# Kernel optimization log

Hardware: AMD Instinct MI355X
Metric: run time of the kernel (lower is better)

The kernel has to match this reference:

```python
import jax, jax.numpy as jnp
import numpy as np

OUT_CHANNELS = 16
IN_CHANNELS = 16
EPS = 1e-8
NEG_SLOPE = 0.1


def setup_inputs() -> dict:
    key = jax.random.key(0)
    k1, _ = jax.random.split(key)
    x = jax.random.normal(k1, (16, IN_CHANNELS, 512, 512), dtype=jnp.float32)
    # default weight from the torch module: pattern - 0.01, flattened to [16]
    pattern = jnp.array([0, 1, 0, 0, 1, 0, 0, 1, 0, 0, 1, 0, 0, 1, 0, 0], dtype=jnp.float32)
    w = pattern - 0.01
    b = jnp.zeros((1,), dtype=jnp.float32)
    return {"x": x, "w": w, "b": b}


def reference(x, w, b):
    # Rolled 1x1 conv: out[:, o] = sum_c w[(c - o) % Cin] * x[:, c] + b
    # (since _roll_tensor(x, o)[c] = x[(c + o) % Cin])
    W2 = jnp.stack([jnp.roll(w, o) for o in range(OUT_CHANNELS)])  # [O, C] circulant
    y = jnp.einsum('bchw,oc->bohw', x, W2) + b[0]
    # leaky_relu(0.1)
    y = jnp.where(y >= 0, y, NEG_SLOPE * y)
    # per (batch, channel) min-max normalize over spatial dims
    mn = jnp.min(y, axis=(2, 3), keepdims=True)
    mx = jnp.max(y, axis=(2, 3), keepdims=True)
    return (y - mn) / (mx - mn + EPS)
```

## Files before the change

kernel.cpp:

```cpp
#include <hip/hip_runtime.h>
#include <math.h>

static constexpr int NB = 16;
static constexpr int NC = 16;
static constexpr int HW = 512 * 512;
static constexpr int V4 = HW / 4;
static constexpr int THREADS = 256;
static constexpr int BLK_PER_B = 128;
static constexpr int ITERS = V4 / (BLK_PER_B * THREADS);
static constexpr int GRID = NB * BLK_PER_B;
static constexpr float NEG_SLOPE = 0.1f;
static constexpr float EPS = 1e-8f;

__device__ __forceinline__ unsigned int fenc(float f) {
    unsigned int u = __float_as_uint(f);
    return (u & 0x80000000u) ? ~u : (u | 0x80000000u);
}
__device__ __forceinline__ float fdec(unsigned int u) {
    u = (u & 0x80000000u) ? (u ^ 0x80000000u) : ~u;
    return __uint_as_float(u);
}

__device__ __forceinline__ float leaky(float v) {
    return v >= 0.0f ? v : NEG_SLOPE * v;
}

template<int PASS>
__global__ __launch_bounds__(THREADS)
void cc_kernel(const float* __restrict__ x, const float* __restrict__ w,
               const float* __restrict__ bptr, unsigned int* __restrict__ mnmx,
               float* __restrict__ out)
{
    const int blk = (PASS == 0) ? blockIdx.x : (GRID - 1 - (int)blockIdx.x);
    const int batch = blk >> 7;
    const int chunk = blk & (BLK_PER_B - 1);
    const float* xb = x + (size_t)batch * NC * HW;

    float wr[16];
    #pragma unroll
    for (int i = 0; i < 16; ++i) wr[i] = w[i];
    const float bias = bptr[0];

    __shared__ float smn[16];
    __shared__ float sscale[16];
    float mn[16], mx[16];

    if (PASS == 0) {
        #pragma unroll
        for (int o = 0; o < 16; ++o) { mn[o] = INFINITY; mx[o] = -INFINITY; }
    } else {
        if (threadIdx.x < 16) {
            const float mnv = fdec(mnmx[batch * 16 + threadIdx.x]);
            const float mxv = fdec(mnmx[256 + batch * 16 + threadIdx.x]);
            smn[threadIdx.x] = mnv;
            sscale[threadIdx.x] = 1.0f / (mxv - mnv + EPS);
        }
        __syncthreads();
    }

    #pragma unroll
    for (int it = 0; it < ITERS; ++it) {
        const int p4 = chunk * (THREADS * ITERS) + it * THREADS + (int)threadIdx.x;
        float4 acc[16];
        #pragma unroll
        for (int o = 0; o < 16; ++o) acc[o] = make_float4(bias, bias, bias, bias);
        #pragma unroll
        for (int c = 0; c < 16; ++c) {
            const float4 xv = reinterpret_cast<const float4*>(xb + (size_t)c * HW)[p4];
            #pragma unroll
            for (int o = 0; o < 16; ++o) {
                const float wc = wr[(c - o) & 15];
                acc[o].x = fmaf(wc, xv.x, acc[o].x);
                acc[o].y = fmaf(wc, xv.y, acc[o].y);
                acc[o].z = fmaf(wc, xv.z, acc[o].z);
                acc[o].w = fmaf(wc, xv.w, acc[o].w);
            }
        }
        #pragma unroll
        for (int o = 0; o < 16; ++o) {
            float4 v = acc[o];
            v.x = leaky(v.x); v.y = leaky(v.y); v.z = leaky(v.z); v.w = leaky(v.w);
            if (PASS == 0) {
                mn[o] = fminf(mn[o], fminf(fminf(v.x, v.y), fminf(v.z, v.w)));
                mx[o] = fmaxf(mx[o], fmaxf(fmaxf(v.x, v.y), fmaxf(v.z, v.w)));
            } else {
                const float m = smn[o], s = sscale[o];
                v.x = (v.x - m) * s; v.y = (v.y - m) * s;
                v.z = (v.z - m) * s; v.w = (v.w - m) * s;
                reinterpret_cast<float4*>(out + (size_t)(batch * NC + o) * HW)[p4] = v;
            }
        }
    }

    if (PASS == 0) {
        #pragma unroll
        for (int o = 0; o < 16; ++o) {
            #pragma unroll
            for (int s = 32; s >= 1; s >>= 1) {
                mn[o] = fminf(mn[o], __shfl_xor(mn[o], s, 64));
                mx[o] = fmaxf(mx[o], __shfl_xor(mx[o], s, 64));
            }
        }
        __shared__ float cmn[4][16], cmx[4][16];
        const int wave = threadIdx.x >> 6;
        const int lane = threadIdx.x & 63;
        if (lane == 0) {
            #pragma unroll
            for (int o = 0; o < 16; ++o) { cmn[wave][o] = mn[o]; cmx[wave][o] = mx[o]; }
        }
        __syncthreads();
        if (threadIdx.x < 16) {
            float v = cmn[0][threadIdx.x];
            #pragma unroll
            for (int wv = 1; wv < 4; ++wv) v = fminf(v, cmn[wv][threadIdx.x]);
            atomicMin(&mnmx[batch * 16 + threadIdx.x], fenc(v));
        } else if (threadIdx.x < 32) {
            const int o = (int)threadIdx.x - 16;
            float v = cmx[0][o];
            #pragma unroll
            for (int wv = 1; wv < 4; ++wv) v = fmaxf(v, cmx[wv][o]);
            atomicMax(&mnmx[256 + batch * 16 + o], fenc(v));
        }
    }
}

extern "C" void kernel_launch(void* const* d_in, const int* in_sizes, int n_in,
                              void* d_out, int out_size, void* d_ws, size_t ws_size,
                              hipStream_t stream) {
    const float* x = (const float*)d_in[0];
    const float* w = (const float*)d_in[1];
    const float* b = (const float*)d_in[2];
    float* out = (float*)d_out;
    unsigned int* mnmx = (unsigned int*)d_ws;

    hipMemsetAsync(mnmx, 0xFF, 256 * sizeof(unsigned int), stream);
    hipMemsetAsync(mnmx + 256, 0x00, 256 * sizeof(unsigned int), stream);

    cc_kernel<0><<<GRID, THREADS, 0, stream>>>(x, w, b, mnmx, out);
    cc_kernel<1><<<GRID, THREADS, 0, stream>>>(x, w, b, mnmx, out);
}
```

Baseline: 506.3 us.

## Replace atomic min/max with partial buffers, reduce kernel, and nontemporal stores

Pass 0 now writes per-block min/max partials to a workspace instead of encoded atomics, and skips leaky ReLU there, since the function is monotonic and can be applied to the reduced extremes. A small reduce kernel combines the partials and precomputes the min and inverse scale, so the two memsets are no longer needed. Pass 1 applies leaky ReLU and normalization and writes the output with nontemporal stores so it does not pollute the cache, which may keep more of x cached for the re-read. The cost is an extra kernel launch and serialization point.

```diff
diff --git a/kernel.cpp b/kernel.cpp
--- a/kernel.cpp
+++ b/kernel.cpp
@@ -12,26 +12,17 @@
 static constexpr float NEG_SLOPE = 0.1f;
 static constexpr float EPS = 1e-8f;
 
-__device__ __forceinline__ unsigned int fenc(float f) {
-    unsigned int u = __float_as_uint(f);
-    return (u & 0x80000000u) ? ~u : (u | 0x80000000u);
-}
-__device__ __forceinline__ float fdec(unsigned int u) {
-    u = (u & 0x80000000u) ? (u ^ 0x80000000u) : ~u;
-    return __uint_as_float(u);
-}
+typedef float f32x4 __attribute__((ext_vector_type(4)));
 
 __device__ __forceinline__ float leaky(float v) {
     return v >= 0.0f ? v : NEG_SLOPE * v;
 }
 
-template<int PASS>
 __global__ __launch_bounds__(THREADS)
-void cc_kernel(const float* __restrict__ x, const float* __restrict__ w,
-               const float* __restrict__ bptr, unsigned int* __restrict__ mnmx,
-               float* __restrict__ out)
+void cc_pass0(const float* __restrict__ x, const float* __restrict__ w,
+              const float* __restrict__ bptr, float* __restrict__ part)
 {
-    const int blk = (PASS == 0) ? blockIdx.x : (GRID - 1 - (int)blockIdx.x);
+    const int blk = blockIdx.x;
     const int batch = blk >> 7;
     const int chunk = blk & (BLK_PER_B - 1);
     const float* xb = x + (size_t)batch * NC * HW;
@@ -41,22 +32,9 @@
     for (int i = 0; i < 16; ++i) wr[i] = w[i];
     const float bias = bptr[0];
 
-    __shared__ float smn[16];
-    __shared__ float sscale[16];
     float mn[16], mx[16];
-
-    if (PASS == 0) {
-        #pragma unroll
-        for (int o = 0; o < 16; ++o) { mn[o] = INFINITY; mx[o] = -INFINITY; }
-    } else {
-        if (threadIdx.x < 16) {
-            const float mnv = fdec(mnmx[batch * 16 + threadIdx.x]);
-            const float mxv = fdec(mnmx[256 + batch * 16 + threadIdx.x]);
-            smn[threadIdx.x] = mnv;
-            sscale[threadIdx.x] = 1.0f / (mxv - mnv + EPS);
-        }
-        __syncthreads();
-    }
+    #pragma unroll
+    for (int o = 0; o < 16; ++o) { mn[o] = INFINITY; mx[o] = -INFINITY; }
 
     #pragma unroll
     for (int it = 0; it < ITERS; ++it) {
@@ -78,48 +56,128 @@
         }
         #pragma unroll
         for (int o = 0; o < 16; ++o) {
-            float4 v = acc[o];
-            v.x = leaky(v.x); v.y = leaky(v.y); v.z = leaky(v.z); v.w = leaky(v.w);
-            if (PASS == 0) {
-                mn[o] = fminf(mn[o], fminf(fminf(v.x, v.y), fminf(v.z, v.w)));
-                mx[o] = fmaxf(mx[o], fmaxf(fmaxf(v.x, v.y), fmaxf(v.z, v.w)));
-            } else {
-                const float m = smn[o], s = sscale[o];
-                v.x = (v.x - m) * s; v.y = (v.y - m) * s;
-                v.z = (v.z - m) * s; v.w = (v.w - m) * s;
-                reinterpret_cast<float4*>(out + (size_t)(batch * NC + o) * HW)[p4] = v;
-            }
+            const float4 v = acc[o];
+            mn[o] = fminf(mn[o], fminf(fminf(v.x, v.y), fminf(v.z, v.w)));
+            mx[o] = fmaxf(mx[o], fmaxf(fmaxf(v.x, v.y), fmaxf(v.z, v.w)));
         }
     }
 
-    if (PASS == 0) {
+    #pragma unroll
+    for (int o = 0; o < 16; ++o) {
+        #pragma unroll
+        for (int s = 32; s >= 1; s >>= 1) {
+            mn[o] = fminf(mn[o], __shfl_xor(mn[o], s, 64));
+            mx[o] = fmaxf(mx[o], __shfl_xor(mx[o], s, 64));
+        }
+    }
+    __shared__ float cmn[4][16], cmx[4][16];
+    const int wave = threadIdx.x >> 6;
+    const int lane = threadIdx.x & 63;
+    if (lane == 0) {
+        #pragma unroll
+        for (int o = 0; o < 16; ++o) { cmn[wave][o] = mn[o]; cmx[wave][o] = mx[o]; }
+    }
+    __syncthreads();
+    if (threadIdx.x < 16) {
+        float v = cmn[0][threadIdx.x];
+        #pragma unroll
+        for (int wv = 1; wv < 4; ++wv) v = fminf(v, cmn[wv][threadIdx.x]);
+        part[(size_t)blk * 32 + threadIdx.x] = v;
+    } else if (threadIdx.x < 32) {
+        const int o = (int)threadIdx.x - 16;
+        float v = cmx[0][o];
+        #pragma unroll
+        for (int wv = 1; wv < 4; ++wv) v = fmaxf(v, cmx[wv][o]);
+        part[(size_t)blk * 32 + threadIdx.x] = v;
+    }
+}
+
+__global__ __launch_bounds__(256)
+void cc_reduce(const float* __restrict__ part, float* __restrict__ fin)
+{
+    const int batch = blockIdx.x;
+    const int t = (int)threadIdx.x;
+    const int slot = t & 31;
+    const int g = t >> 5;
+    const bool isMin = slot < 16;
+    float v = isMin ? INFINITY : -INFINITY;
+    #pragma unroll
+    for (int i = 0; i < BLK_PER_B / 8; ++i) {
+        const int c = g * (BLK_PER_B / 8) + i;
+        const float p = part[((size_t)batch * BLK_PER_B + c) * 32 + slot];
+        v = isMin ? fminf(v, p) : fmaxf(v, p);
+    }
+    __shared__ float red[8][32];
+    red[g][slot] = v;
+    __syncthreads();
+    if (t < 32) {
+        float r = red[0][slot];
+        #pragma unroll
+        for (int i = 1; i < 8; ++i)
+            r = isMin ? fminf(r, red[i][slot]) : fmaxf(r, red[i][slot]);
+        red[0][slot] = r;
+    }
+    __syncthreads();
+    if (t < 16) {
+        const float mnL = leaky(red[0][t]);
+        const float mxL = leaky(red[0][16 + t]);
+        fin[batch * 32 + t] = mnL;
+        fin[batch * 32 + 16 + t] = 1.0f / (mxL - mnL + EPS);
+    }
+}
+
+__global__ __launch_bounds__(THREADS)
+void cc_pass1(const float* __restrict__ x, const float* __restrict__ w,
+              const float* __restrict__ bptr, const float* __restrict__ fin,
+              float* __restrict__ out)
+{
+    const int blk = GRID - 1 - (int)blockIdx.x;
+    const int batch = blk >> 7;
+    const int chunk = blk & (BLK_PER_B - 1);
+    const float* xb = x + (size_t)batch * NC * HW;
+
+    float wr[16];
+    #pragma unroll
+    for (int i = 0; i < 16; ++i) wr[i] = w[i];
+    const float bias = bptr[0];
+
+    __shared__ float smn[16];
+    __shared__ float sscale[16];
+    if (threadIdx.x < 16) {
+        smn[threadIdx.x] = fin[batch * 32 + threadIdx.x];
+    } else if (threadIdx.x < 32) {
+        sscale[threadIdx.x - 16] = fin[batch * 32 + threadIdx.x];
+    }
+    __syncthreads();
+
+    #pragma unroll
+    for (int it = 0; it < ITERS; ++it) {
+        const int p4 = chunk * (THREADS * ITERS) + it * THREADS + (int)threadIdx.x;
+        float4 acc[16];
+        #pragma unroll
+        for (int o = 0; o < 16; ++o) acc[o] = make_float4(bias, bias, bias, bias);
+        #pragma unroll
+        for (int c = 0; c < 16; ++c) {
+            const float4 xv = reinterpret_cast<const float4*>(xb + (size_t)c * HW)[p4];
+            #pragma unroll
+            for (int o = 0; o < 16; ++o) {
+                const float wc = wr[(c - o) & 15];
+                acc[o].x = fmaf(wc, xv.x, acc[o].x);
+                acc[o].y = fmaf(wc, xv.y, acc[o].y);
+                acc[o].z = fmaf(wc, xv.z, acc[o].z);
+                acc[o].w = fmaf(wc, xv.w, acc[o].w);
+            }
+        }
         #pragma unroll
         for (int o = 0; o < 16; ++o) {
-            #pragma unroll
-            for (int s = 32; s >= 1; s >>= 1) {
-                mn[o] = fminf(mn[o], __shfl_xor(mn[o], s, 64));
-                mx[o] = fmaxf(mx[o], __shfl_xor(mx[o], s, 64));
-            }
-        }
-        __shared__ float cmn[4][16], cmx[4][16];
-        const int wave = threadIdx.x >> 6;
-        const int lane = threadIdx.x & 63;
-        if (lane == 0) {
-            #pragma unroll
-            for (int o = 0; o < 16; ++o) { cmn[wave][o] = mn[o]; cmx[wave][o] = mx[o]; }
-        }
-        __syncthreads();
-        if (threadIdx.x < 16) {
-            float v = cmn[0][threadIdx.x];
-            #pragma unroll
-            for (int wv = 1; wv < 4; ++wv) v = fminf(v, cmn[wv][threadIdx.x]);
-            atomicMin(&mnmx[batch * 16 + threadIdx.x], fenc(v));
-        } else if (threadIdx.x < 32) {
-            const int o = (int)threadIdx.x - 16;
-            float v = cmx[0][o];
-            #pragma unroll
-            for (int wv = 1; wv < 4; ++wv) v = fmaxf(v, cmx[wv][o]);
-            atomicMax(&mnmx[256 + batch * 16 + o], fenc(v));
+            const float m = smn[o], s = sscale[o];
+            f32x4 v;
+            v.x = (leaky(acc[o].x) - m) * s;
+            v.y = (leaky(acc[o].y) - m) * s;
+            v.z = (leaky(acc[o].z) - m) * s;
+            v.w = (leaky(acc[o].w) - m) * s;
+            f32x4* dst = reinterpret_cast<f32x4*>(out + (size_t)(batch * NC + o) * HW) + p4;
+            __builtin_nontemporal_store(v, dst);
         }
     }
 }
@@ -131,11 +189,10 @@
     const float* w = (const float*)d_in[1];
     const float* b = (const float*)d_in[2];
     float* out = (float*)d_out;
-    unsigned int* mnmx = (unsigned int*)d_ws;
+    float* part = (float*)d_ws;
+    float* fin  = (float*)d_ws + (size_t)GRID * 32;
 
-    hipMemsetAsync(mnmx, 0xFF, 256 * sizeof(unsigned int), stream);
-    hipMemsetAsync(mnmx + 256, 0x00, 256 * sizeof(unsigned int), stream);
-
-    cc_kernel<0><<<GRID, THREADS, 0, stream>>>(x, w, b, mnmx, out);
-    cc_kernel<1><<<GRID, THREADS, 0, stream>>>(x, w, b, mnmx, out);
+    cc_pass0<<<GRID, THREADS, 0, stream>>>(x, w, b, part);
+    cc_reduce<<<NB, 256, 0, stream>>>(part, fin);
+    cc_pass1<<<GRID, THREADS, 0, stream>>>(x, w, b, fin, out);
 }
```

After: 488.3 us. 1.04x faster.
